# Performance work log

Hardware: AMD Instinct MI355X
Metric: run time of the kernel (lower is better)

Reference implementation:

```python
import jax, jax.numpy as jnp
import numpy as np
import math

A = 32; B = 32; PSIZE = 16; K = 3; STRIDE = 2; PAD = 1; ITERS = 3; FINAL_LAMBDA = 0.01
KK = K * K; KKA = KK * A; KKA2 = KKA // 2 + 1
EPS = 1e-12; LN2PI = math.log(2 * math.pi)


def unfold(x, k, s, p):
    # torch F.unfold: output feature dim ordered (C, kh, kw), columns row-major
    b, C, h, w = x.shape
    xp = jnp.pad(x, ((0, 0), (0, 0), (p, p), (p, p)))
    oh = (h + 2 * p - k) // s + 1
    ow = (w + 2 * p - k) // s + 1
    cols = [xp[:, :, ki:ki + s * (oh - 1) + 1:s, kj:kj + s * (ow - 1) + 1:s]
            for ki in range(k) for kj in range(k)]
    patches = jnp.stack(cols, axis=2)  # [b, C, kk, oh, ow]
    return patches.reshape(b, C, k * k, oh * ow), oh, ow


def setup_inputs():
    key = jax.random.key(0)
    ks = jax.random.split(key, 8)
    b, h, w = 4, 14, 14
    a_in = jax.random.uniform(ks[0], (b, A, h, w), dtype=jnp.float32)
    pose = jax.random.normal(ks[1], (b, A * PSIZE, h, w), dtype=jnp.float32)
    mpose_w = jax.random.normal(ks[2], (B * PSIZE, PSIZE), dtype=jnp.float32) / np.float32(np.sqrt(PSIZE))
    mpose_b = jnp.zeros((B * PSIZE,), jnp.float32)
    freq_w = jax.random.normal(ks[3], (KKA2, PSIZE, 2), dtype=jnp.float32) * 0.02
    ln_g = jnp.ones((A,), jnp.float32)
    ln_b = jnp.zeros((A,), jnp.float32)
    lim = np.float32(np.sqrt(6.0 / (KK + KK)))  # xavier_uniform on [kk, kk, 1]
    spat_w = jax.random.uniform(ks[4], (KK, KK, 1), jnp.float32, -lim, lim)
    spat_bias = jnp.ones((KK,), jnp.float32)
    beta_u = jnp.zeros((1, 1, B, 1), jnp.float32)
    beta_a = jnp.zeros((1, 1, B), jnp.float32)
    return dict(a_in=a_in, pose=pose, mpose_w=mpose_w, mpose_b=mpose_b,
                freq_w=freq_w, ln_g=ln_g, ln_b=ln_b, spat_w=spat_w,
                spat_bias=spat_bias, beta_u=beta_u, beta_a=beta_a)


def _forward(a_in, pose, mpose_w, mpose_b, freq_w, ln_g, ln_b,
             spat_w, spat_bias, beta_u, beta_a):
    b = a_in.shape[0]
    pose_u, oh, ow = unfold(pose, K, STRIDE, PAD)  # [b, A*PSIZE, KK, l]
    l = oh * ow
    pose_u = pose_u.reshape(b, A, PSIZE, KK, l)
    pose_u = pose_u.transpose(0, 4, 3, 1, 2).reshape(b, l, KKA, PSIZE)
    # mpose linear: psize -> B*psize
    po = jnp.einsum('blkp,qp->blkq', pose_u, mpose_w) + mpose_b
    po = po.reshape(b * l, KKA, B, PSIZE)
    # Frequency FFT filter over kkA axis (weight shared across all B slices)
    xf = jnp.fft.rfft(po, axis=1, norm='ortho')        # [bl, KKA2, B, PSIZE] complex
    wc = freq_w[..., 0] + 1j * freq_w[..., 1]           # [KKA2, PSIZE]
    xf = xf * wc[None, :, None, :]
    po = jnp.fft.irfft(xf, n=KKA, axis=1, norm='ortho') + po  # residual
    v = po.reshape(b, l, KKA, B, PSIZE)
    a_u, _, _ = unfold(a_in, K, STRIDE, PAD)            # [b, A, KK, l]
    a_u = a_u.transpose(0, 3, 2, 1).reshape(b, l, KKA)
    # Spatial gating applied to ones-initialized r (identical for every B slice)
    ones = jnp.ones((b * l, KKA), jnp.float32)
    g = ones.reshape(b * l, KK, A)
    mu_g = g.mean(-1, keepdims=True)
    var_g = ((g - mu_g) ** 2).mean(-1, keepdims=True)
    gn = (g - mu_g) / jnp.sqrt(var_g + 1e-5) * ln_g + ln_b
    g2 = jnp.einsum('ij,nja->nia', spat_w[:, :, 0], gn) + spat_bias[None, :, None]
    gate = jax.nn.gelu(g2, approximate=False).reshape(b * l, KKA) + ones
    logit = jnp.broadcast_to(gate[:, :, None], (b * l, KKA, B))
    r = jax.nn.softmax(logit, axis=2).reshape(b, l, KKA, B, 1)
    a_out = mu = None
    for i in range(ITERS):
        lam = FINAL_LAMBDA * (1.0 - 0.95 ** (i + 1))
        # m-step
        rr = r * a_u[:, :, :, None, None]
        r_sum = rr.sum(axis=2, keepdims=True)                 # [b,l,1,B,1]
        coeff = rr / (r_sum + EPS)
        mu = (coeff * v).sum(axis=2, keepdims=True)           # [b,l,1,B,PSIZE]
        sig = (coeff * (v - mu) ** 2).sum(axis=2, keepdims=True) + EPS
        cost = (beta_u + jnp.log(jnp.sqrt(sig[:, :, 0]))) * r_sum[:, :, 0]  # [b,l,B,PSIZE]
        a_out = jax.nn.sigmoid(lam * (beta_a - cost.sum(axis=3)))           # [b,l,B]
        if i < ITERS - 1:
            # e-step (note: log(sigma_sq * ln2pi) is faithful to the original code)
            ln_p = (-0.5 * jnp.sum(jnp.log(sig * LN2PI), axis=-1)
                    - jnp.sum((v - mu) ** 2 / (2.0 * sig), axis=-1))        # [b,l,KKA,B]
            ln_ap = ln_p + jnp.log(a_out[:, :, None, :])
            r = jax.nn.softmax(ln_ap, axis=-1)[..., None]
    pose_out = mu[:, :, 0].reshape(b, l, B * PSIZE).transpose(0, 2, 1).reshape(b, B * PSIZE, oh, ow)
    a_fin = a_out.transpose(0, 2, 1).reshape(b, B, oh, ow)
    return a_fin, pose_out


def reference(a_in, pose, mpose_w, mpose_b, freq_w, ln_g, ln_b,
              spat_w, spat_bias, beta_u, beta_a):
    return _forward(a_in, pose, mpose_w, mpose_b, freq_w, ln_g, ln_b,
                    spat_w, spat_bias, beta_u, beta_a)
```

## Files before the change

kernel.cpp:

```cpp
#include <hip/hip_runtime.h>
#include <hip/hip_bf16.h>
#include <math.h>

#define A_    32
#define B_    32
#define PS    16
#define KK_   9
#define KKA_  288
#define OH_   7
#define L_    49
#define NB    4
#define NSITE 196
#define NCOLS 3136

#define LAM1 5.0e-4f
#define LAM2 9.75e-4f
#define LAM3 1.42625e-3f
#define LOG_LN2PI 0.6086775903077413f

#define DSTR 33

typedef _Float16 half2v __attribute__((ext_vector_type(2)));
typedef short    short8 __attribute__((ext_vector_type(8)));
typedef float    floatx4 __attribute__((ext_vector_type(4)));

static __device__ __forceinline__ float san(float x, float lo, float hi){
    return fminf(fmaxf(x, lo), hi);
}

static __device__ __forceinline__ float dot2acc(half2v a, half2v b, float c){
#if __has_builtin(__builtin_amdgcn_fdot2)
    return __builtin_amdgcn_fdot2(a, b, c, false);
#else
    return c + (float)a.x*(float)b.x + (float)a.y*(float)b.y;
#endif
}

__global__ void k_prep(const float* __restrict__ fw, const float* __restrict__ pose,
                       ushort* __restrict__ cpr, float* __restrict__ csum,
                       __hip_bfloat16* __restrict__ Xt, int nc)
{
    if ((int)blockIdx.x < nc){
        int id = (int)blockIdx.x*256 + threadIdx.x;
        if (id >= 16*288) return;
        int p = id / 288, m = id % 288;
        float acc = fw[(0*16 + p)*2 + 0];
        for (int k = 1; k <= 143; ++k){
            float re = fw[(k*16 + p)*2 + 0];
            float im = fw[(k*16 + p)*2 + 1];
            int km = (k*m) % 288;
            float ang = 0.021816615649929116f * (float)km;
            float s, c; __sincosf(ang, &s, &c);
            acc += 2.0f*(re*c - im*s);
        }
        float re144 = fw[(144*16 + p)*2 + 0];
        acc += re144 * ((m & 1) ? -1.0f : 1.0f);
        float cv = acc * (1.0f/288.0f);
        if (m == 0) cv += 1.0f;
        cv = san(cv, -1e4f, 1e4f);

        __hip_bfloat16 hb = __float2bfloat16(cv);
        float hif = __bfloat162float(hb);
        __hip_bfloat16 lb = __float2bfloat16(cv - hif);
        ushort hi = *(ushort*)&hb, lo = *(ushort*)&lb;

        ushort* c0h = cpr + p*592;
        ushort* c1h = cpr + 16*592   + p*592;
        ushort* c0l = cpr + 16*592*2 + p*592;
        ushort* c1l = cpr + 16*592*3 + p*592;
        int x1 = 288 - m;
        c0h[x1] = hi;  c0l[x1] = lo;
        c1h[x1-1] = hi; c1l[x1-1] = lo;
        if (m >= 1){
            int x2 = 576 - m;
            c0h[x2] = hi;  c0l[x2] = lo;
            c1h[x2-1] = hi; c1l[x2-1] = lo;
        } else {
            c0h[0] = hi; c0l[0] = lo;
            csum[p] = san(1.0f + fw[(0*16 + p)*2 + 0], -1e4f, 1e4f);
        }
        return;
    }
    int id = ((int)blockIdx.x - nc)*256 + threadIdx.x;
    if (id >= NCOLS*KKA_/8) return;
    int c = id / (KKA_/8), j8 = id % (KKA_/8);
    int j = j8*8;
    int n = c >> 4, q = c & 15;
    int bs = n / L_, l = n % L_, oy = l / OH_, ox = l % OH_;
    int kk = j >> 5, a0 = j & 31;
    int y = oy*2 - 1 + kk/3, x = ox*2 - 1 + kk%3;
    const bool inb = ((unsigned)y < 14u && (unsigned)x < 14u);
    const float* psrc = pose + (((long)bs*(A_*PS))*14 + y)*14 + x;
    union { ushort us[8]; uint4 u4; } res;
    #pragma unroll
    for (int u = 0; u < 8; ++u){
        float v = 0.f;
        if (inb) v = psrc[((a0+u)*PS + q)*196];
        __hip_bfloat16 hb = __float2bfloat16(san(v, -1e4f, 1e4f));
        res.us[u] = *(ushort*)&hb;
    }
    *(uint4*)&Xt[c*KKA_ + j] = res.u4;
}

__launch_bounds__(512, 1)
__global__ void
k_mega(const ushort* __restrict__ cpr, const __hip_bfloat16* __restrict__ Xt,
       const float* __restrict__ a_in,
       const float* __restrict__ mpw, const float* __restrict__ mpb,
       const float* __restrict__ csum,
       const float* __restrict__ beta_u, const float* __restrict__ beta_a,
       uint* __restrict__ vg,
       float* __restrict__ out)
{
    const int nl = blockIdx.x;
    const int t = threadIdx.x;
    const int Bc = t >> 4, p = t & 15;
    const int bs = nl / L_, l = nl % L_;

    __shared__ __align__(16) _Float16 us[2*4224];
    __shared__ float dall[288*DSTR];
    __shared__ float a_s[KKA_];
    __shared__ float cst[32];

    uint* const vgs = vg + (long)nl*144*512 + t;

    for (int j = t; j < KKA_; j += 512){
        int kk = j >> 5, a = j & 31;
        int oy = l / OH_, ox = l % OH_;
        int y = oy*2 - 1 + kk/3, x = ox*2 - 1 + kk%3;
        float v = 0.f;
        if ((unsigned)y < 14u && (unsigned)x < 14u)
            v = a_in[((bs*A_ + a)*14 + y)*14 + x];
        a_s[j] = san(v, 0.f, 1e4f);
    }
    half2v w_h[8];
    #pragma unroll
    for (int k = 0; k < 8; ++k){
        w_h[k].x = (_Float16)mpw[t*16 + 2*k];
        w_h[k].y = (_Float16)mpw[t*16 + 2*k + 1];
    }
    const float vb = mpb[t] * csum[p];
    const float bu = beta_u[Bc];
    const float ba = beta_a[Bc];
    __syncthreads();

    float s0a = 0.f, s0b = 0.f, s0c = 0.f, s0d = 0.f;
    for (int j = 0; j < KKA_; j += 4){
        s0a += a_s[j]; s0b += a_s[j+1]; s0c += a_s[j+2]; s0d += a_s[j+3];
    }
    const float S0tot = (s0a + s0b) + (s0c + s0d);

    const int w = t >> 6, lane = t & 63;
    const int mn = lane & 15, quad = lane >> 4;
    const int p0 = w*2;
    const __hip_bfloat16* xrow = Xt + (nl*16 + mn)*KKA_ + quad*8;

    float S1 = 0.f, S2 = 0.f;

    auto do_chunk = [&](int ch, _Float16* usb){
        floatx4 accA = {0,0,0,0}, accB = {0,0,0,0};
        for (int k0i = 0; k0i < 9; ++k0i){
            const int k0 = k0i*32;
            short8 bfrag = *(const short8*)&xrow[k0];
            #pragma unroll
            for (int pp = 0; pp < 2; ++pp){
                const int pg = p0 + pp;
                int o = 288 + k0 + quad*8 - (ch*16 + mn);
                int sel = o & 1, off = o - sel;
                const ushort* bh = cpr + (sel ? 16*592 : 0) + pg*592;
                const ushort* bl = cpr + 16*592*2 + (sel ? 16*592 : 0) + pg*592;
                short8 ah = *(const short8*)&bh[off];
                short8 al = *(const short8*)&bl[off];
                floatx4 acc = pp ? accB : accA;
                acc = __builtin_amdgcn_mfma_f32_16x16x32_bf16(ah, bfrag, acc, 0, 0, 0);
                acc = __builtin_amdgcn_mfma_f32_16x16x32_bf16(al, bfrag, acc, 0, 0, 0);
                if (pp) accB = acc; else accA = acc;
            }
        }
        #pragma unroll
        for (int r = 0; r < 4; ++r){
            usb[p0*264     + (quad*4 + r)*16 + mn] = (_Float16)accA[r];
            usb[(p0+1)*264 + (quad*4 + r)*16 + mn] = (_Float16)accB[r];
        }
    };

    auto vpair = [&](const _Float16* urow, int s, float& v0o, float& v1o){
        union { uint4 u4; half2v h2[4]; } A0, A1, B0, B1;
        A0.u4 = *(const uint4*)&urow[(2*s)*16];
        A1.u4 = *(const uint4*)&urow[(2*s)*16 + 8];
        B0.u4 = *(const uint4*)&urow[(2*s+1)*16];
        B1.u4 = *(const uint4*)&urow[(2*s+1)*16 + 8];
        float v0 = vb, v1 = vb;
        #pragma unroll
        for (int m = 0; m < 4; ++m){
            v0 = dot2acc(A0.h2[m], w_h[m],   v0);
            v0 = dot2acc(A1.h2[m], w_h[4+m], v0);
            v1 = dot2acc(B0.h2[m], w_h[m],   v1);
            v1 = dot2acc(B1.h2[m], w_h[4+m], v1);
        }
        v0o = v0; v1o = v1;
    };

    for (int ch = 0; ch < 18; ++ch){
        _Float16* usb = us + (ch & 1)*4224;
        do_chunk(ch, usb);
        __syncthreads();
        const _Float16* urow = &usb[p*264];
        #pragma unroll
        for (int s = 0; s < 8; ++s){
            float v0, v1; vpair(urow, s, v0, v1);
            const int i0 = ch*16 + 2*s;
            const float a0 = a_s[i0], a1 = a_s[i0+1];
            S1 += a0*v0 + a1*v1;
            S2 += a0*v0*v0 + a1*v1*v1;
            union { half2v h; uint u; } cv;
            cv.h.x = (_Float16)v0; cv.h.y = (_Float16)v1;
            vgs[(ch*8 + s)*512] = cv.u;
        }
    }

    float mu_r, i2s_r;
    {
        const float rs  = S0tot * (1.0f/32.0f);
        const float inv = 1.0f / (rs + 1e-12f);
        const float S1r = S1 * (1.0f/32.0f), S2r = S2 * (1.0f/32.0f);
        mu_r = S1r * inv;
        const float sg  = fmaxf((S2r - 2.f*mu_r*S1r + mu_r*mu_r*rs) * inv, 0.f) + 1e-12f;
        i2s_r = 0.5f / sg;
        const float lg  = logf(sg);
        float cs = (bu + 0.5f*lg) * rs;
        float ls = lg + LOG_LN2PI;
        #pragma unroll
        for (int m = 1; m < 16; m <<= 1){ cs += __shfl_xor(cs, m, 16); ls += __shfl_xor(ls, m, 16); }
        const float aout = san(1.f/(1.f + expf(-LAM1*(ba - cs))), 1e-30f, 1.f);
        if (p == 0) cst[Bc] = logf(aout) - 0.5f*ls;
    }
    __syncthreads();

    const int b0 = p & 1, b1 = (p>>1)&1, b2 = (p>>2)&1, b3 = (p>>3)&1;
    const int isub = t >> 5, Bce = t & 31;
    float muF = 0.f, aF = 0.f;
    for (int it = 0; it < 2; ++it){
        const float lam = it ? LAM3 : LAM2;

        auto dtree = [&](int ibase, const uint* uu){
            float e1[8], e2[4], e3[2], dfin;
            #pragma unroll
            for (int s = 0; s < 8; ++s){
                union { uint u; half2v h; } cv; cv.u = uu[s];
                float v0 = (float)cv.h.x, v1 = (float)cv.h.y;
                float d0 = v0 - mu_r, d1 = v1 - mu_r;
                float ea = d0*d0*i2s_r, eb = d1*d1*i2s_r;
                float aown  = b0 ? eb : ea;
                float asend = b0 ? ea : eb;
                e1[s] = aown + __shfl_xor(asend, 1);
            }
            #pragma unroll
            for (int s = 0; s < 4; ++s){
                float aown  = b1 ? e1[2*s+1] : e1[2*s];
                float asend = b1 ? e1[2*s]   : e1[2*s+1];
                e2[s] = aown + __shfl_xor(asend, 2);
            }
            #pragma unroll
            for (int s = 0; s < 2; ++s){
                float aown  = b2 ? e2[2*s+1] : e2[2*s];
                float asend = b2 ? e2[2*s]   : e2[2*s+1];
                e3[s] = aown + __shfl_xor(asend, 4);
            }
            {
                float aown  = b3 ? e3[1] : e3[0];
                float asend = b3 ? e3[0] : e3[1];
                dfin = aown + __shfl_xor(asend, 8);
            }
            dall[(ibase + p)*DSTR + Bc] = dfin;
        };
        for (int g = 0; g < 18; ++g){
            uint uu[8];
            #pragma unroll
            for (int s = 0; s < 8; ++s) uu[s] = vgs[(g*8 + s)*512];
            dtree(g*16, uu);
        }
        __syncthreads();

        {
            const float cb = cst[Bce];
            #pragma unroll
            for (int g = 0; g < 18; ++g){
                float* dp = &dall[(g*16 + isub)*DSTR + Bce];
                float lnap = cb - *dp;
                float mx = lnap;
                #pragma unroll
                for (int m = 16; m >= 1; m >>= 1) mx = fmaxf(mx, __shfl_xor(mx, m));
                float ex = expf(lnap - mx);
                float sm = ex;
                #pragma unroll
                for (int m = 16; m >= 1; m >>= 1) sm += __shfl_xor(sm, m);
                *dp = (ex / sm) * a_s[g*16 + isub];
            }
        }
        __syncthreads();

        float T0 = 0.f, T1 = 0.f, T2 = 0.f;
        auto csum3 = [&](int ibase, const uint* uu){
            #pragma unroll
            for (int s = 0; s < 8; ++s){
                union { uint u; half2v h; } cv; cv.u = uu[s];
                float v0 = (float)cv.h.x, v1 = (float)cv.h.y;
                float r0 = dall[(ibase + 2*s)*DSTR + Bc];
                float r1 = dall[(ibase + 2*s + 1)*DSTR + Bc];
                T0 += r0 + r1;
                T1 += r0*v0 + r1*v1;
                T2 += r0*v0*v0 + r1*v1*v1;
            }
        };
        for (int g = 0; g < 18; ++g){
            uint uu[8];
            #pragma unroll
            for (int s = 0; s < 8; ++s) uu[s] = vgs[(g*8 + s)*512];
            csum3(g*16, uu);
        }

        const float inv = 1.f/(T0 + 1e-12f);
        const float mu  = T1 * inv;
        const float sg  = fmaxf((T2 - 2.f*mu*T1 + mu*mu*T0) * inv, 0.f) + 1e-12f;
        const float lg  = logf(sg);
        float cs = (bu + 0.5f*lg) * T0;
        float ls = lg + LOG_LN2PI;
        #pragma unroll
        for (int m = 1; m < 16; m <<= 1){ cs += __shfl_xor(cs, m, 16); ls += __shfl_xor(ls, m, 16); }
        const float aout = san(1.f/(1.f + expf(-lam*(ba - cs))), 1e-30f, 1.f);
        if (it == 0){
            mu_r = mu; i2s_r = 0.5f/sg;
            if (p == 0) cst[Bc] = logf(aout) - 0.5f*ls;
            __syncthreads();
        } else { muF = mu; aF = aout; }
    }

    if (p == 0) out[bs*(B_*L_) + Bc*L_ + l] = san(aF, 0.f, 1.f);
    out[6272 + (bs*512 + t)*L_ + l] = san(muF, -1e4f, 1e4f);
}

extern "C" void kernel_launch(void* const* d_in, const int* in_sizes, int n_in,
                              void* d_out, int out_size, void* d_ws, size_t ws_size,
                              hipStream_t stream)
{
    const float* a_in   = (const float*)d_in[0];
    const float* pose   = (const float*)d_in[1];
    const float* mpw    = (const float*)d_in[2];
    const float* mpb    = (const float*)d_in[3];
    const float* fw     = (const float*)d_in[4];
    const float* beta_u = (const float*)d_in[9];
    const float* beta_a = (const float*)d_in[10];
    float* out = (float*)d_out;

    char* base = (char*)d_ws;
    float*  csum = (float*)(base + 0);
    ushort* cpr  = (ushort*)(base + 256);
    __hip_bfloat16* Xt = (__hip_bfloat16*)(base + 76288);
    uint*   vg   = (uint*)(base + 1882624);

    const int nc = 18;
    const int nx = (NCOLS*KKA_/8 + 255)/256;
    k_prep<<<nc + nx, 256, 0, stream>>>(fw, pose, cpr, csum, Xt, nc);
    k_mega<<<NSITE, 512, 0, stream>>>(cpr, Xt, a_in, mpw, mpb, csum, beta_u, beta_a, vg, out);
}
```

Before: 268.0 us.

## Double k_mega threads to 1024 and stage pose im2col through shared memory

k_mega now runs 1024 threads per site, split into two halves. Each MFMA wave handles a single p-group, and each half processes half of the s/g loop ranges. Partial sums from the two halves are combined through new shared buffers, which adds extra barriers. k_prep's im2col pass now loads a per-(batch,q) pose slab into LDS as bf16 and gathers coalesced 8-element packs, replacing strided global reads across thousands of small blocks. The goals are more latency hiding on a grid of only 196 blocks and cheaper pose gathering, at the cost of higher LDS use and register pressure under the 1024 launch bound.

Result: slower. 323.9 us (+20.8%).

```diff
diff --git a/kernel.cpp b/kernel.cpp
--- a/kernel.cpp
+++ b/kernel.cpp
@@ -40,6 +40,7 @@
                        ushort* __restrict__ cpr, float* __restrict__ csum,
                        __hip_bfloat16* __restrict__ Xt, int nc)
 {
+    __shared__ ushort pl[32][200];
     if ((int)blockIdx.x < nc){
         int id = (int)blockIdx.x*256 + threadIdx.x;
         if (id >= 16*288) return;
@@ -81,28 +82,34 @@
         }
         return;
     }
-    int id = ((int)blockIdx.x - nc)*256 + threadIdx.x;
-    if (id >= NCOLS*KKA_/8) return;
-    int c = id / (KKA_/8), j8 = id % (KKA_/8);
-    int j = j8*8;
-    int n = c >> 4, q = c & 15;
-    int bs = n / L_, l = n % L_, oy = l / OH_, ox = l % OH_;
-    int kk = j >> 5, a0 = j & 31;
-    int y = oy*2 - 1 + kk/3, x = ox*2 - 1 + kk%3;
-    const bool inb = ((unsigned)y < 14u && (unsigned)x < 14u);
-    const float* psrc = pose + (((long)bs*(A_*PS))*14 + y)*14 + x;
-    union { ushort us[8]; uint4 u4; } res;
-    #pragma unroll
-    for (int u = 0; u < 8; ++u){
-        float v = 0.f;
-        if (inb) v = psrc[((a0+u)*PS + q)*196];
+    int id2 = (int)blockIdx.x - nc;
+    int bs = id2 >> 4, q = id2 & 15;
+    int tid = threadIdx.x;
+    for (int e = tid; e < 32*196; e += 256){
+        int a = e / 196, yx = e % 196;
+        float v = pose[(bs*512 + a*16 + q)*196 + yx];
         __hip_bfloat16 hb = __float2bfloat16(san(v, -1e4f, 1e4f));
-        res.us[u] = *(ushort*)&hb;
-    }
-    *(uint4*)&Xt[c*KKA_ + j] = res.u4;
-}
-
-__launch_bounds__(512, 1)
+        pl[a][yx] = *(ushort*)&hb;
+    }
+    __syncthreads();
+    for (int idx = tid; idx < 49*9*4; idx += 256){
+        int l = idx / 36, r2 = idx % 36, kk = r2 >> 2, a8 = r2 & 3;
+        int oy = l / 7, ox = l % 7;
+        int y = oy*2 - 1 + kk/3, x = ox*2 - 1 + kk%3;
+        int cc = (bs*49 + l)*16 + q;
+        union { ushort us8[8]; uint4 u4; } res;
+        if ((unsigned)y < 14u && (unsigned)x < 14u){
+            int yx = y*14 + x;
+            #pragma unroll
+            for (int u = 0; u < 8; ++u) res.us8[u] = pl[a8*8 + u][yx];
+        } else {
+            res.u4.x = 0; res.u4.y = 0; res.u4.z = 0; res.u4.w = 0;
+        }
+        *(uint4*)&Xt[cc*KKA_ + kk*32 + a8*8] = res.u4;
+    }
+}
+
+__launch_bounds__(1024, 1)
 __global__ void
 k_mega(const ushort* __restrict__ cpr, const __hip_bfloat16* __restrict__ Xt,
        const float* __restrict__ a_in,
@@ -114,17 +121,22 @@
 {
     const int nl = blockIdx.x;
     const int t = threadIdx.x;
-    const int Bc = t >> 4, p = t & 15;
+    const int c = t & 511;
+    const int h = t >> 9;
+    const int Bc = c >> 4, p = c & 15;
     const int bs = nl / L_, l = nl % L_;
 
     __shared__ __align__(16) _Float16 us[2*4224];
     __shared__ float dall[288*DSTR];
     __shared__ float a_s[KKA_];
     __shared__ float cst[32];
-
-    uint* const vgs = vg + (long)nl*144*512 + t;
-
-    for (int j = t; j < KKA_; j += 512){
+    __shared__ float tred[3*512];
+    __shared__ float mub[512];
+    __shared__ float i2b[512];
+
+    uint* const vgs = vg + (long)nl*144*512 + c;
+
+    for (int j = t; j < KKA_; j += 1024){
         int kk = j >> 5, a = j & 31;
         int oy = l / OH_, ox = l % OH_;
         int y = oy*2 - 1 + kk/3, x = ox*2 - 1 + kk%3;
@@ -136,10 +148,10 @@
     half2v w_h[8];
     #pragma unroll
     for (int k = 0; k < 8; ++k){
-        w_h[k].x = (_Float16)mpw[t*16 + 2*k];
-        w_h[k].y = (_Float16)mpw[t*16 + 2*k + 1];
-    }
-    const float vb = mpb[t] * csum[p];
+        w_h[k].x = (_Float16)mpw[c*16 + 2*k];
+        w_h[k].y = (_Float16)mpw[c*16 + 2*k + 1];
+    }
+    const float vb = mpb[c] * csum[p];
     const float bu = beta_u[Bc];
     const float ba = beta_a[Bc];
     __syncthreads();
@@ -150,38 +162,29 @@
     }
     const float S0tot = (s0a + s0b) + (s0c + s0d);
 
-    const int w = t >> 6, lane = t & 63;
+    const int pg = t >> 6, lane = t & 63;
     const int mn = lane & 15, quad = lane >> 4;
-    const int p0 = w*2;
     const __hip_bfloat16* xrow = Xt + (nl*16 + mn)*KKA_ + quad*8;
 
     float S1 = 0.f, S2 = 0.f;
 
     auto do_chunk = [&](int ch, _Float16* usb){
-        floatx4 accA = {0,0,0,0}, accB = {0,0,0,0};
+        floatx4 acc = {0,0,0,0};
         for (int k0i = 0; k0i < 9; ++k0i){
             const int k0 = k0i*32;
             short8 bfrag = *(const short8*)&xrow[k0];
-            #pragma unroll
-            for (int pp = 0; pp < 2; ++pp){
-                const int pg = p0 + pp;
-                int o = 288 + k0 + quad*8 - (ch*16 + mn);
-                int sel = o & 1, off = o - sel;
-                const ushort* bh = cpr + (sel ? 16*592 : 0) + pg*592;
-                const ushort* bl = cpr + 16*592*2 + (sel ? 16*592 : 0) + pg*592;
-                short8 ah = *(const short8*)&bh[off];
-                short8 al = *(const short8*)&bl[off];
-                floatx4 acc = pp ? accB : accA;
-                acc = __builtin_amdgcn_mfma_f32_16x16x32_bf16(ah, bfrag, acc, 0, 0, 0);
-                acc = __builtin_amdgcn_mfma_f32_16x16x32_bf16(al, bfrag, acc, 0, 0, 0);
-                if (pp) accB = acc; else accA = acc;
-            }
+            int o = 288 + k0 + quad*8 - (ch*16 + mn);
+            int sel = o & 1, off = o - sel;
+            const ushort* bh = cpr + (sel ? 16*592 : 0) + pg*592;
+            const ushort* bl = cpr + 16*592*2 + (sel ? 16*592 : 0) + pg*592;
+            short8 ah = *(const short8*)&bh[off];
+            short8 al = *(const short8*)&bl[off];
+            acc = __builtin_amdgcn_mfma_f32_16x16x32_bf16(ah, bfrag, acc, 0, 0, 0);
+            acc = __builtin_amdgcn_mfma_f32_16x16x32_bf16(al, bfrag, acc, 0, 0, 0);
         }
         #pragma unroll
-        for (int r = 0; r < 4; ++r){
-            usb[p0*264     + (quad*4 + r)*16 + mn] = (_Float16)accA[r];
-            usb[(p0+1)*264 + (quad*4 + r)*16 + mn] = (_Float16)accB[r];
-        }
+        for (int r = 0; r < 4; ++r)
+            usb[pg*264 + (quad*4 + r)*16 + mn] = (_Float16)acc[r];
     };
 
     auto vpair = [&](const _Float16* urow, int s, float& v0o, float& v1o){
@@ -207,26 +210,30 @@
         __syncthreads();
         const _Float16* urow = &usb[p*264];
         #pragma unroll
-        for (int s = 0; s < 8; ++s){
+        for (int s4 = 0; s4 < 4; ++s4){
+            const int s = h*4 + s4;
             float v0, v1; vpair(urow, s, v0, v1);
             const int i0 = ch*16 + 2*s;
             const float a0 = a_s[i0], a1 = a_s[i0+1];
             S1 += a0*v0 + a1*v1;
             S2 += a0*v0*v0 + a1*v1*v1;
-            union { half2v h; uint u; } cv;
-            cv.h.x = (_Float16)v0; cv.h.y = (_Float16)v1;
+            union { half2v hh; uint u; } cv;
+            cv.hh.x = (_Float16)v0; cv.hh.y = (_Float16)v1;
             vgs[(ch*8 + s)*512] = cv.u;
         }
     }
 
+    if (h == 1){ tred[c] = S1; tred[512 + c] = S2; }
+    __syncthreads();
     float mu_r, i2s_r;
-    {
+    if (h == 0){
+        const float S1t = S1 + tred[c];
+        const float S2t = S2 + tred[512 + c];
         const float rs  = S0tot * (1.0f/32.0f);
         const float inv = 1.0f / (rs + 1e-12f);
-        const float S1r = S1 * (1.0f/32.0f), S2r = S2 * (1.0f/32.0f);
-        mu_r = S1r * inv;
-        const float sg  = fmaxf((S2r - 2.f*mu_r*S1r + mu_r*mu_r*rs) * inv, 0.f) + 1e-12f;
-        i2s_r = 0.5f / sg;
+        const float S1r = S1t * (1.0f/32.0f), S2r = S2t * (1.0f/32.0f);
+        const float mu  = S1r * inv;
+        const float sg  = fmaxf((S2r - 2.f*mu*S1r + mu*mu*rs) * inv, 0.f) + 1e-12f;
         const float lg  = logf(sg);
         float cs = (bu + 0.5f*lg) * rs;
         float ls = lg + LOG_LN2PI;
@@ -234,11 +241,13 @@
         for (int m = 1; m < 16; m <<= 1){ cs += __shfl_xor(cs, m, 16); ls += __shfl_xor(ls, m, 16); }
         const float aout = san(1.f/(1.f + expf(-LAM1*(ba - cs))), 1e-30f, 1.f);
         if (p == 0) cst[Bc] = logf(aout) - 0.5f*ls;
+        mub[c] = mu; i2b[c] = 0.5f/sg;
     }
     __syncthreads();
+    mu_r = mub[c]; i2s_r = i2b[c];
 
     const int b0 = p & 1, b1 = (p>>1)&1, b2 = (p>>2)&1, b3 = (p>>3)&1;
-    const int isub = t >> 5, Bce = t & 31;
+    const int isub2 = t >> 5, Bce = t & 31;
     float muF = 0.f, aF = 0.f;
     for (int it = 0; it < 2; ++it){
         const float lam = it ? LAM3 : LAM2;
@@ -247,8 +256,8 @@
             float e1[8], e2[4], e3[2], dfin;
             #pragma unroll
             for (int s = 0; s < 8; ++s){
-                union { uint u; half2v h; } cv; cv.u = uu[s];
-                float v0 = (float)cv.h.x, v1 = (float)cv.h.y;
+                union { uint u; half2v hh; } cv; cv.u = uu[s];
+                float v0 = (float)cv.hh.x, v1 = (float)cv.hh.y;
                 float d0 = v0 - mu_r, d1 = v1 - mu_r;
                 float ea = d0*d0*i2s_r, eb = d1*d1*i2s_r;
                 float aown  = b0 ? eb : ea;
@@ -274,7 +283,8 @@
             }
             dall[(ibase + p)*DSTR + Bc] = dfin;
         };
-        for (int g = 0; g < 18; ++g){
+        for (int g2 = 0; g2 < 9; ++g2){
+            const int g = h*9 + g2;
             uint uu[8];
             #pragma unroll
             for (int s = 0; s < 8; ++s) uu[s] = vgs[(g*8 + s)*512];
@@ -285,8 +295,8 @@
         {
             const float cb = cst[Bce];
             #pragma unroll
-            for (int g = 0; g < 18; ++g){
-                float* dp = &dall[(g*16 + isub)*DSTR + Bce];
+            for (int g2 = 0; g2 < 9; ++g2){
+                float* dp = &dall[(g2*32 + isub2)*DSTR + Bce];
                 float lnap = cb - *dp;
                 float mx = lnap;
                 #pragma unroll
@@ -295,49 +305,58 @@
                 float sm = ex;
                 #pragma unroll
                 for (int m = 16; m >= 1; m >>= 1) sm += __shfl_xor(sm, m);
-                *dp = (ex / sm) * a_s[g*16 + isub];
+                *dp = (ex / sm) * a_s[g2*32 + isub2];
             }
         }
         __syncthreads();
 
         float T0 = 0.f, T1 = 0.f, T2 = 0.f;
-        auto csum3 = [&](int ibase, const uint* uu){
+        for (int g2 = 0; g2 < 9; ++g2){
+            const int g = h*9 + g2;
+            const int ibase = g*16;
+            uint uu[8];
+            #pragma unroll
+            for (int s = 0; s < 8; ++s) uu[s] = vgs[(g*8 + s)*512];
             #pragma unroll
             for (int s = 0; s < 8; ++s){
-                union { uint u; half2v h; } cv; cv.u = uu[s];
-                float v0 = (float)cv.h.x, v1 = (float)cv.h.y;
+                union { uint u; half2v hh; } cv; cv.u = uu[s];
+                float v0 = (float)cv.hh.x, v1 = (float)cv.hh.y;
                 float r0 = dall[(ibase + 2*s)*DSTR + Bc];
                 float r1 = dall[(ibase + 2*s + 1)*DSTR + Bc];
                 T0 += r0 + r1;
                 T1 += r0*v0 + r1*v1;
                 T2 += r0*v0*v0 + r1*v1*v1;
             }
-        };
-        for (int g = 0; g < 18; ++g){
-            uint uu[8];
-            #pragma unroll
-            for (int s = 0; s < 8; ++s) uu[s] = vgs[(g*8 + s)*512];
-            csum3(g*16, uu);
-        }
-
-        const float inv = 1.f/(T0 + 1e-12f);
-        const float mu  = T1 * inv;
-        const float sg  = fmaxf((T2 - 2.f*mu*T1 + mu*mu*T0) * inv, 0.f) + 1e-12f;
-        const float lg  = logf(sg);
-        float cs = (bu + 0.5f*lg) * T0;
-        float ls = lg + LOG_LN2PI;
-        #pragma unroll
-        for (int m = 1; m < 16; m <<= 1){ cs += __shfl_xor(cs, m, 16); ls += __shfl_xor(ls, m, 16); }
-        const float aout = san(1.f/(1.f + expf(-lam*(ba - cs))), 1e-30f, 1.f);
+        }
+        if (h == 1){ tred[c] = T0; tred[512 + c] = T1; tred[1024 + c] = T2; }
+        __syncthreads();
+
+        if (h == 0){
+            T0 += tred[c]; T1 += tred[512 + c]; T2 += tred[1024 + c];
+            const float inv = 1.f/(T0 + 1e-12f);
+            const float mu  = T1 * inv;
+            const float sg  = fmaxf((T2 - 2.f*mu*T1 + mu*mu*T0) * inv, 0.f) + 1e-12f;
+            const float lg  = logf(sg);
+            float cs = (bu + 0.5f*lg) * T0;
+            float ls = lg + LOG_LN2PI;
+            #pragma unroll
+            for (int m = 1; m < 16; m <<= 1){ cs += __shfl_xor(cs, m, 16); ls += __shfl_xor(ls, m, 16); }
+            const float aout = san(1.f/(1.f + expf(-lam*(ba - cs))), 1e-30f, 1.f);
+            if (it == 0){
+                mub[c] = mu; i2b[c] = 0.5f/sg;
+                if (p == 0) cst[Bc] = logf(aout) - 0.5f*ls;
+            } else { muF = mu; aF = aout; }
+        }
         if (it == 0){
-            mu_r = mu; i2s_r = 0.5f/sg;
-            if (p == 0) cst[Bc] = logf(aout) - 0.5f*ls;
             __syncthreads();
-        } else { muF = mu; aF = aout; }
-    }
-
-    if (p == 0) out[bs*(B_*L_) + Bc*L_ + l] = san(aF, 0.f, 1.f);
-    out[6272 + (bs*512 + t)*L_ + l] = san(muF, -1e4f, 1e4f);
+            mu_r = mub[c]; i2s_r = i2b[c];
+        }
+    }
+
+    if (h == 0){
+        if (p == 0) out[bs*(B_*L_) + Bc*L_ + l] = san(aF, 0.f, 1.f);
+        out[6272 + (bs*512 + c)*L_ + l] = san(muF, -1e4f, 1e4f);
+    }
 }
 
 extern "C" void kernel_launch(void* const* d_in, const int* in_sizes, int n_in,
@@ -360,7 +379,6 @@
     uint*   vg   = (uint*)(base + 1882624);
 
     const int nc = 18;
-    const int nx = (NCOLS*KKA_/8 + 255)/256;
-    k_prep<<<nc + nx, 256, 0, stream>>>(fw, pose, cpr, csum, Xt, nc);
-    k_mega<<<NSITE, 512, 0, stream>>>(cpr, Xt, a_in, mpw, mpb, csum, beta_u, beta_a, vg, out);
-}
+    k_prep<<<nc + 64, 256, 0, stream>>>(fw, pose, cpr, csum, Xt, nc);
+    k_mega<<<NSITE, 1024, 0, stream>>>(cpr, Xt, a_in, mpw, mpb, csum, beta_u, beta_a, vg, out);
+}
```
